# Kernel optimization log

Hardware: AMD Instinct MI355X
Metric: run time of the kernel (lower is better)

The kernel has to match this reference:

```python
import jax, jax.numpy as jnp
import numpy as np

B, H, W, C = 4, 64, 64, 512
EPS = 1e-3  # keras BatchNormalization default epsilon


def setup_inputs() -> dict:
    key = jax.random.key(0)
    ks = jax.random.split(key, 16)
    c8, c2 = C // 8, C // 2
    sc = lambda fan_in: 1.0 / np.sqrt(fan_in)
    inp = {
        "x": jax.random.normal(ks[0], (B, H, W, C), dtype=jnp.float32),
        # 1x1 conv weights as [Cin, Cout] matrices
        "wf": jax.random.normal(ks[1], (C, c8), dtype=jnp.float32) * sc(C),
        "bf": jnp.zeros((c8,), jnp.float32),
        "wg": jax.random.normal(ks[2], (C, c8), dtype=jnp.float32) * sc(C),
        "bg": jnp.zeros((c8,), jnp.float32),
        "wh": jax.random.normal(ks[3], (C, c2), dtype=jnp.float32) * sc(C),
        "bh": jnp.zeros((c2,), jnp.float32),
        "wo": jax.random.normal(ks[4], (c2, C), dtype=jnp.float32) * sc(c2),
        "bo": jnp.zeros((C,), jnp.float32),
        "gamma": jax.random.normal(ks[5], (1,), dtype=jnp.float32) * 0.05,
        # concat 1x1 conv (2C -> C), has bias (use_batchnorm=False default)
        "wc": jax.random.normal(ks[6], (2 * C, C), dtype=jnp.float32) * sc(2 * C),
        "bc": jnp.zeros((C,), jnp.float32),
        # BN inference params (moving statistics)
        "bn_scale": jnp.ones((C,), jnp.float32),
        "bn_bias": jnp.zeros((C,), jnp.float32),
        "bn_mean": jnp.zeros((C,), jnp.float32),
        "bn_var": jnp.ones((C,), jnp.float32),
    }
    return inp


def reference(x, wf, bf, wg, bg, wh, bh, wo, bo, gamma, wc, bc,
              bn_scale, bn_bias, bn_mean, bn_var):
    b, h, w, c = x.shape
    n = h * w
    xf = x.reshape(b, n, c)
    f = xf @ wf + bf          # [B, N, C/8]
    g = xf @ wg + bg          # [B, N, C/8]
    hv = xf @ wh + bh         # [B, N, C/2]
    s = jnp.einsum('bnd,bmd->bnm', g, f)   # [B, N, N]
    beta = jax.nn.softmax(s, axis=-1)
    o = jnp.einsum('bnm,bmd->bnd', beta, hv)  # [B, N, C/2]
    o = o @ wo + bo                            # [B, N, C]
    att = gamma * o + xf                       # gamma-scaled residual
    cat = jnp.concatenate([att, xf], axis=-1)  # [B, N, 2C]
    y = cat @ wc + bc
    # BatchNorm inference + relu
    y = (y - bn_mean) * (bn_scale / jnp.sqrt(bn_var + EPS)) + bn_bias
    y = jax.nn.relu(y)
    return y.reshape(b, h, w, c)
```

## Files before the change

kernel.cpp:

```cpp
#include <hip/hip_runtime.h>
#include <hip/hip_bf16.h>

typedef __bf16 bf16x8 __attribute__((ext_vector_type(8)));
typedef float f32x4 __attribute__((ext_vector_type(4)));

#define EPSBN 1e-3f

constexpr int NPIX = 4096;
constexpr int D2 = 256;

__global__ __launch_bounds__(256) void k_cvt(const float* __restrict__ x,
                                             __bf16* __restrict__ xb, int n4) {
  int i = blockIdx.x * 256 + threadIdx.x;
  if (i >= n4) return;
  float4 v = reinterpret_cast<const float4*>(x)[i];
  union { __bf16 h[4]; uint2 u; } o;
  o.h[0] = (__bf16)v.x; o.h[1] = (__bf16)v.y; o.h[2] = (__bf16)v.z; o.h[3] = (__bf16)v.w;
  reinterpret_cast<uint2*>(xb)[i] = o.u;
}

__global__ __launch_bounds__(256) void kp_wfgh(const float* __restrict__ wf,
                                               const float* __restrict__ wg,
                                               const float* __restrict__ wh,
                                               __bf16* __restrict__ WT) {
  int idx = blockIdx.x * 256 + threadIdx.x;
  int c = idx >> 9, k = idx & 511;
  float v = (c < 64) ? wf[k * 64 + c] : (c < 128) ? wg[k * 64 + (c - 64)] : wh[k * 256 + (c - 128)];
  WT[idx] = (__bf16)v;
}

__global__ __launch_bounds__(128) void kp_bias384(const float* bf_, const float* bg_,
                                                  const float* bh_, float* bias) {
  int c = blockIdx.x * 128 + threadIdx.x;
  bias[c] = (c < 64) ? bf_[c] : (c < 128) ? bg_[c - 64] : bh_[c - 128];
}

__global__ __launch_bounds__(256) void kp_wow(const float* __restrict__ wo,
                                              const float* __restrict__ wc,
                                              float* __restrict__ Wow) {
  int idx = blockIdx.x * 256 + threadIdx.x;
  int d = idx >> 9, c = idx & 511;
  float acc = 0.f;
  for (int j = 0; j < 512; ++j) acc += wo[d * 512 + j] * wc[j * 512 + c];
  Wow[idx] = acc;
}

__global__ __launch_bounds__(256) void kp_wcat(const float* __restrict__ Wow,
                                               const float* __restrict__ wc,
                                               const float* __restrict__ gamma,
                                               const float* __restrict__ bns,
                                               const float* __restrict__ bnv,
                                               __bf16* __restrict__ WT) {
  int idx = blockIdx.x * 256 + threadIdx.x;
  int c = idx / 768, k = idx % 768;
  float s = bns[c] * rsqrtf(bnv[c] + EPSBN);
  float v;
  if (k < 256) v = gamma[0] * Wow[k * 512 + c] * s;
  else { int kk = k - 256; v = (wc[kk * 512 + c] + wc[(512 + kk) * 512 + c]) * s; }
  WT[idx] = (__bf16)v;
}

__global__ __launch_bounds__(256) void kp_biasF(const float* bo, const float* wc, const float* bc,
                                                const float* gamma, const float* bns, const float* bnb,
                                                const float* bnm, const float* bnv, float* biasF) {
  int c = blockIdx.x * 256 + threadIdx.x;
  float s = bns[c] * rsqrtf(bnv[c] + EPSBN);
  float acc = 0.f;
  for (int j = 0; j < 512; ++j) acc += bo[j] * wc[j * 512 + c];
  float pre = bc[c] + gamma[0] * acc;
  biasF[c] = (pre - bnm[c]) * s + bnb[c];
}

template <int KT, int NC, bool FINAL>
__global__ __launch_bounds__(256) void k_gemm(const __bf16* __restrict__ A1, int k1, int lda1,
                                              const __bf16* __restrict__ A2, int lda2,
                                              const __bf16* __restrict__ WT,
                                              const float* __restrict__ bias,
                                              void* __restrict__ outp) {
  __shared__ __bf16 As[128][72];
  __shared__ __bf16 Ws[64][72];
  const int m0 = blockIdx.x * 128, n0 = blockIdx.y * 64;
  const int tid = threadIdx.x, lane = tid & 63, w = tid >> 6;
  const int wr = w >> 1, wcl = w & 1;
  const int l15 = lane & 15, l4 = lane >> 4;
  f32x4 acc[4][2] = {};
  for (int ks = 0; ks < KT; ks += 64) {
    const __bf16* Asrc; int lda, kb;
    if (ks < k1) { Asrc = A1; lda = lda1; kb = ks; }
    else         { Asrc = A2; lda = lda2; kb = ks - k1; }
#pragma unroll
    for (int it = 0; it < 4; ++it) {
      int idx = it * 256 + tid, r = idx >> 3, ch = idx & 7;
      *(bf16x8*)(&As[r][ch * 8]) = *(const bf16x8*)(Asrc + (size_t)(m0 + r) * lda + kb + ch * 8);
    }
#pragma unroll
    for (int it = 0; it < 2; ++it) {
      int idx = it * 256 + tid, r = idx >> 3, ch = idx & 7;
      *(bf16x8*)(&Ws[r][ch * 8]) = *(const bf16x8*)(WT + (size_t)(n0 + r) * KT + ks + ch * 8);
    }
    __syncthreads();
#pragma unroll
    for (int kk = 0; kk < 2; ++kk) {
      int krd = kk * 32 + l4 * 8;
      bf16x8 av[4], bv[2];
#pragma unroll
      for (int mi = 0; mi < 4; ++mi) av[mi] = *(const bf16x8*)(&As[wr * 64 + mi * 16 + l15][krd]);
#pragma unroll
      for (int ni = 0; ni < 2; ++ni) bv[ni] = *(const bf16x8*)(&Ws[wcl * 32 + ni * 16 + l15][krd]);
#pragma unroll
      for (int mi = 0; mi < 4; ++mi)
#pragma unroll
        for (int ni = 0; ni < 2; ++ni)
          acc[mi][ni] = __builtin_amdgcn_mfma_f32_16x16x32_bf16(av[mi], bv[ni], acc[mi][ni], 0, 0, 0);
    }
    __syncthreads();
  }
#pragma unroll
  for (int mi = 0; mi < 4; ++mi)
#pragma unroll
    for (int ni = 0; ni < 2; ++ni) {
      int col = n0 + wcl * 32 + ni * 16 + l15;
      float bcol = bias[col];
#pragma unroll
      for (int r = 0; r < 4; ++r) {
        int row = m0 + wr * 64 + mi * 16 + l4 * 4 + r;
        float v = acc[mi][ni][r] + bcol;
        if (FINAL) ((float*)outp)[(size_t)row * NC + col] = fmaxf(v, 0.f);
        else ((__bf16*)outp)[(size_t)row * NC + col] = (__bf16)v;
      }
    }
}

__global__ __launch_bounds__(256) void k_trans(const __bf16* __restrict__ fgh,
                                               __bf16* __restrict__ hvT) {
  __shared__ __bf16 T[64][72];
  int b = blockIdx.z, n0 = blockIdx.x * 64, d0 = blockIdx.y * 64;
  int tid = threadIdx.x;
  const __bf16* src = fgh + (size_t)b * NPIX * 384;
#pragma unroll
  for (int it = 0; it < 2; ++it) {
    int idx = it * 256 + tid, r = idx >> 3, ch = idx & 7;
    *(bf16x8*)(&T[r][ch * 8]) = *(const bf16x8*)(src + (size_t)(n0 + r) * 384 + 128 + d0 + ch * 8);
  }
  __syncthreads();
  __bf16* dst = hvT + ((size_t)b * D2 + d0) * NPIX + n0;
#pragma unroll
  for (int it = 0; it < 2; ++it) {
    int idx = it * 256 + tid, r = idx >> 3, ch = idx & 7;
    bf16x8 v;
#pragma unroll
    for (int j = 0; j < 8; ++j) v[j] = T[ch * 8 + j][r];
    *(bf16x8*)(dst + (size_t)r * NPIX + ch * 8) = v;
  }
}

__global__ __launch_bounds__(256, 2) void k_attn(const __bf16* __restrict__ fgh,
                                                 const __bf16* __restrict__ hvT,
                                                 __bf16* __restrict__ obuf) {
  __shared__ __bf16 Fs[64][72];
  __shared__ __bf16 Vs[256][72];
  __shared__ __bf16 Ps[32][72];
  __shared__ float Lp[4][32];
  const int b = blockIdx.y, q0 = blockIdx.x * 32;
  const int tid = threadIdx.x, w = tid >> 6, lane = tid & 63;
  const int l15 = lane & 15, l4 = lane >> 4;
  const __bf16* base = fgh + (size_t)b * NPIX * 384;
  const __bf16* vbase = hvT + (size_t)b * D2 * NPIX;
  bf16x8 aG[2][2];
#pragma unroll
  for (int qi = 0; qi < 2; ++qi)
#pragma unroll
    for (int kk = 0; kk < 2; ++kk)
      aG[qi][kk] = *(const bf16x8*)(base + (size_t)(q0 + qi * 16 + l15) * 384 + 64 + kk * 32 + l4 * 8);
  f32x4 accO[2][4] = {};
  f32x4 lsum[2] = {};
  for (int m0 = 0; m0 < NPIX; m0 += 64) {
#pragma unroll
    for (int it = 0; it < 2; ++it) {
      int idx = it * 256 + tid, r = idx >> 3, ch = idx & 7;
      *(bf16x8*)(&Fs[r][ch * 8]) = *(const bf16x8*)(base + (size_t)(m0 + r) * 384 + ch * 8);
    }
#pragma unroll
    for (int it = 0; it < 8; ++it) {
      int idx = it * 256 + tid, r = idx >> 3, ch = idx & 7;
      *(bf16x8*)(&Vs[r][ch * 8]) = *(const bf16x8*)(vbase + (size_t)r * NPIX + m0 + ch * 8);
    }
    __syncthreads();
#pragma unroll
    for (int qi = 0; qi < 2; ++qi) {
      f32x4 sa = {};
#pragma unroll
      for (int kk = 0; kk < 2; ++kk) {
        bf16x8 bF = *(const bf16x8*)(&Fs[w * 16 + l15][kk * 32 + l4 * 8]);
        sa = __builtin_amdgcn_mfma_f32_16x16x32_bf16(aG[qi][kk], bF, sa, 0, 0, 0);
      }
#pragma unroll
      for (int r = 0; r < 4; ++r) {
        float p = __expf(sa[r]);
        lsum[qi][r] += p;
        Ps[qi * 16 + l4 * 4 + r][w * 16 + l15] = (__bf16)p;
      }
    }
    __syncthreads();
#pragma unroll
    for (int kk = 0; kk < 2; ++kk) {
      bf16x8 aP[2];
#pragma unroll
      for (int qi = 0; qi < 2; ++qi) aP[qi] = *(const bf16x8*)(&Ps[qi * 16 + l15][kk * 32 + l4 * 8]);
#pragma unroll
      for (int dj = 0; dj < 4; ++dj) {
        bf16x8 bV = *(const bf16x8*)(&Vs[w * 64 + dj * 16 + l15][kk * 32 + l4 * 8]);
#pragma unroll
        for (int qi = 0; qi < 2; ++qi)
          accO[qi][dj] = __builtin_amdgcn_mfma_f32_16x16x32_bf16(aP[qi], bV, accO[qi][dj], 0, 0, 0);
      }
    }
    __syncthreads();
  }
#pragma unroll
  for (int qi = 0; qi < 2; ++qi)
#pragma unroll
    for (int r = 0; r < 4; ++r) {
      float v = lsum[qi][r];
      v += __shfl_xor(v, 1); v += __shfl_xor(v, 2); v += __shfl_xor(v, 4); v += __shfl_xor(v, 8);
      lsum[qi][r] = v;
    }
  if (l15 == 0) {
#pragma unroll
    for (int qi = 0; qi < 2; ++qi)
#pragma unroll
      for (int r = 0; r < 4; ++r) Lp[w][qi * 16 + l4 * 4 + r] = lsum[qi][r];
  }
  __syncthreads();
  __bf16* out = obuf + ((size_t)b * NPIX + q0) * D2;
#pragma unroll
  for (int qi = 0; qi < 2; ++qi)
#pragma unroll
    for (int r = 0; r < 4; ++r) {
      int q = qi * 16 + l4 * 4 + r;
      float lt = Lp[0][q] + Lp[1][q] + Lp[2][q] + Lp[3][q];
      float inv = 1.0f / lt;
#pragma unroll
      for (int dj = 0; dj < 4; ++dj)
        out[(size_t)q * D2 + w * 64 + dj * 16 + l15] = (__bf16)(accO[qi][dj][r] * inv);
    }
}

extern "C" void kernel_launch(void* const* d_in, const int* in_sizes, int n_in,
                              void* d_out, int out_size, void* d_ws, size_t ws_size,
                              hipStream_t stream) {
  const float* x = (const float*)d_in[0];
  const float* wf = (const float*)d_in[1];
  const float* bf_ = (const float*)d_in[2];
  const float* wg = (const float*)d_in[3];
  const float* bg_ = (const float*)d_in[4];
  const float* wh = (const float*)d_in[5];
  const float* bh_ = (const float*)d_in[6];
  const float* wo = (const float*)d_in[7];
  const float* bo = (const float*)d_in[8];
  const float* gamma = (const float*)d_in[9];
  const float* wc = (const float*)d_in[10];
  const float* bc = (const float*)d_in[11];
  const float* bns = (const float*)d_in[12];
  const float* bnb = (const float*)d_in[13];
  const float* bnm = (const float*)d_in[14];
  const float* bnv = (const float*)d_in[15];
  (void)in_sizes; (void)n_in; (void)out_size; (void)ws_size;

  char* ws = (char*)d_ws;
  __bf16* xb     = (__bf16*)(ws + 0);
  __bf16* fgh    = (__bf16*)(ws + 16777216);
  __bf16* hvT    = (__bf16*)(ws + 29360128);
  __bf16* obuf   = (__bf16*)(ws + 37748736);
  __bf16* WfghT  = (__bf16*)(ws + 46137344);
  float*  bias384= (float*) (ws + 46530560);
  float*  Wow    = (float*) (ws + 46532096);
  __bf16* WcatT  = (__bf16*)(ws + 47056384);
  float*  biasF  = (float*) (ws + 47842816);
  float* out = (float*)d_out;

  hipLaunchKernelGGL(k_cvt, dim3(8192), dim3(256), 0, stream, x, xb, 2097152);
  hipLaunchKernelGGL(kp_wfgh, dim3(768), dim3(256), 0, stream, wf, wg, wh, WfghT);
  hipLaunchKernelGGL(kp_bias384, dim3(3), dim3(128), 0, stream, bf_, bg_, bh_, bias384);
  hipLaunchKernelGGL(kp_wow, dim3(512), dim3(256), 0, stream, wo, wc, Wow);
  hipLaunchKernelGGL(kp_wcat, dim3(1536), dim3(256), 0, stream, Wow, wc, gamma, bns, bnv, WcatT);
  hipLaunchKernelGGL(kp_biasF, dim3(2), dim3(256), 0, stream, bo, wc, bc, gamma, bns, bnb, bnm, bnv, biasF);
  hipLaunchKernelGGL((k_gemm<512, 384, false>), dim3(128, 6), dim3(256), 0, stream,
                     xb, 512, 512, xb, 512, WfghT, bias384, (void*)fgh);
  hipLaunchKernelGGL(k_trans, dim3(64, 4, 4), dim3(256), 0, stream, fgh, hvT);
  hipLaunchKernelGGL(k_attn, dim3(128, 4), dim3(256), 0, stream, fgh, hvT, obuf);
  hipLaunchKernelGGL((k_gemm<768, 512, true>), dim3(128, 8), dim3(256), 0, stream,
                     obuf, 256, 256, xb, 512, WcatT, biasF, (void*)out);
}
```

Measured before the change: 302.4 us.

## Fuse hv transpose into projection GEMM and restructure attention to register-resident operands

The projection GEMM now writes f/g into a compact 128-wide buffer and writes hv directly transposed, which removes the separate transpose kernel and its extra pass over memory. The attention kernel is rewritten to use 512 threads per 64-query block. It keeps F and V fragments in registers, prefetched from global memory one tile ahead, instead of staging them through shared memory. Only the probability tile goes through a double-buffered LDS array, synchronised by a single raw barrier per step, and blocks are mapped so each XCD handles one batch. The cost is higher register pressure, scattered 8-byte transposed stores in the GEMM epilogue, and a reliance on L2 for the repeated global fragment loads.

Result: faster. 278.4 us (-7.9%).

```diff
diff --git a/kernel.cpp b/kernel.cpp
--- a/kernel.cpp
+++ b/kernel.cpp
@@ -8,6 +8,12 @@
 
 constexpr int NPIX = 4096;
 constexpr int D2 = 256;
+
+#define RAW_BARRIER() do { \
+  asm volatile("s_waitcnt lgkmcnt(0)" ::: "memory"); \
+  __builtin_amdgcn_s_barrier(); \
+  asm volatile("" ::: "memory"); \
+} while (0)
 
 __global__ __launch_bounds__(256) void k_cvt(const float* __restrict__ x,
                                              __bf16* __restrict__ xb, int n4) {
@@ -71,12 +77,13 @@
   biasF[c] = (pre - bnm[c]) * s + bnb[c];
 }
 
-template <int KT, int NC, bool FINAL>
+template <int KT, int NC, int MODE>
 __global__ __launch_bounds__(256) void k_gemm(const __bf16* __restrict__ A1, int k1, int lda1,
                                               const __bf16* __restrict__ A2, int lda2,
                                               const __bf16* __restrict__ WT,
                                               const float* __restrict__ bias,
-                                              void* __restrict__ outp) {
+                                              void* __restrict__ out1,
+                                              void* __restrict__ out2) {
   __shared__ __bf16 As[128][72];
   __shared__ __bf16 Ws[64][72];
   const int m0 = blockIdx.x * 128, n0 = blockIdx.y * 64;
@@ -121,129 +128,142 @@
     for (int ni = 0; ni < 2; ++ni) {
       int col = n0 + wcl * 32 + ni * 16 + l15;
       float bcol = bias[col];
-#pragma unroll
-      for (int r = 0; r < 4; ++r) {
-        int row = m0 + wr * 64 + mi * 16 + l4 * 4 + r;
-        float v = acc[mi][ni][r] + bcol;
-        if (FINAL) ((float*)outp)[(size_t)row * NC + col] = fmaxf(v, 0.f);
-        else ((__bf16*)outp)[(size_t)row * NC + col] = (__bf16)v;
+      int row0 = m0 + wr * 64 + mi * 16 + l4 * 4;
+      if (MODE == 1) {
+        float* out = (float*)out1;
+#pragma unroll
+        for (int r = 0; r < 4; ++r)
+          out[(size_t)(row0 + r) * NC + col] = fmaxf(acc[mi][ni][r] + bcol, 0.f);
+      } else {
+        if (col < 128) {
+          __bf16* fg = (__bf16*)out1;
+#pragma unroll
+          for (int r = 0; r < 4; ++r)
+            fg[(size_t)(row0 + r) * 128 + col] = (__bf16)(acc[mi][ni][r] + bcol);
+        } else {
+          __bf16* hvT = (__bf16*)out2;
+          int bb = row0 >> 12, n = row0 & 4095;
+          union { __bf16 h[4]; uint2 u; } pk;
+#pragma unroll
+          for (int r = 0; r < 4; ++r) pk.h[r] = (__bf16)(acc[mi][ni][r] + bcol);
+          *(uint2*)(hvT + ((size_t)(bb * 256 + (col - 128))) * 4096 + n) = pk.u;
+        }
       }
     }
 }
 
-__global__ __launch_bounds__(256) void k_trans(const __bf16* __restrict__ fgh,
-                                               __bf16* __restrict__ hvT) {
-  __shared__ __bf16 T[64][72];
-  int b = blockIdx.z, n0 = blockIdx.x * 64, d0 = blockIdx.y * 64;
-  int tid = threadIdx.x;
-  const __bf16* src = fgh + (size_t)b * NPIX * 384;
-#pragma unroll
-  for (int it = 0; it < 2; ++it) {
-    int idx = it * 256 + tid, r = idx >> 3, ch = idx & 7;
-    *(bf16x8*)(&T[r][ch * 8]) = *(const bf16x8*)(src + (size_t)(n0 + r) * 384 + 128 + d0 + ch * 8);
+__global__ __launch_bounds__(512, 2) void k_attn(const __bf16* __restrict__ fg,
+                                                 const __bf16* __restrict__ hvT,
+                                                 __bf16* __restrict__ obuf) {
+  __shared__ __bf16 PsT[2][64][136];
+  __shared__ float Lp[8][64];
+  const int id = blockIdx.x;
+  const int xcd = id & 7, i2 = id >> 3;
+  const int b = xcd >> 1;
+  const int q0 = (i2 * 2 + (xcd & 1)) * 64;
+  const int tid = threadIdx.x, w = tid >> 6, lane = tid & 63;
+  const int l15 = lane & 15, l4 = lane >> 4;
+  const __bf16* fgb = fg + (size_t)b * NPIX * 128;
+  const __bf16* vb = hvT + (size_t)b * D2 * NPIX;
+
+  bf16x8 bG[4][2];
+#pragma unroll
+  for (int qt = 0; qt < 4; ++qt)
+#pragma unroll
+    for (int kk = 0; kk < 2; ++kk)
+      bG[qt][kk] = *(const bf16x8*)(fgb + (size_t)(q0 + qt * 16 + l15) * 128 + 64 + kk * 32 + l4 * 8);
+
+  bf16x8 aF[2], bV[2][4];
+#pragma unroll
+  for (int kk = 0; kk < 2; ++kk)
+    aF[kk] = *(const bf16x8*)(fgb + (size_t)(w * 16 + l15) * 128 + kk * 32 + l4 * 8);
+#pragma unroll
+  for (int dj = 0; dj < 2; ++dj)
+#pragma unroll
+    for (int k4 = 0; k4 < 4; ++k4)
+      bV[dj][k4] = *(const bf16x8*)(vb + (size_t)(w * 32 + dj * 16 + l15) * NPIX + k4 * 32 + l4 * 8);
+
+  f32x4 accO[4][2] = {};
+  float lsum[4] = {0.f, 0.f, 0.f, 0.f};
+
+  for (int t = 0; t < 32; ++t) {
+    const int mn = ((t + 1) * 128) & (NPIX - 1);
+    const int bufi = t & 1;
+    f32x4 s[4];
+#pragma unroll
+    for (int qt = 0; qt < 4; ++qt) {
+      s[qt] = (f32x4){0.f, 0.f, 0.f, 0.f};
+#pragma unroll
+      for (int kk = 0; kk < 2; ++kk)
+        s[qt] = __builtin_amdgcn_mfma_f32_16x16x32_bf16(aF[kk], bG[qt][kk], s[qt], 0, 0, 0);
+    }
+    bf16x8 aFn[2];
+#pragma unroll
+    for (int kk = 0; kk < 2; ++kk)
+      aFn[kk] = *(const bf16x8*)(fgb + (size_t)(mn + w * 16 + l15) * 128 + kk * 32 + l4 * 8);
+#pragma unroll
+    for (int qt = 0; qt < 4; ++qt) {
+      float p0 = __expf(s[qt][0]), p1 = __expf(s[qt][1]);
+      float p2 = __expf(s[qt][2]), p3 = __expf(s[qt][3]);
+      lsum[qt] += (p0 + p1) + (p2 + p3);
+      union { __bf16 h[2]; uint u; } w0, w1;
+      w0.h[0] = (__bf16)p0; w0.h[1] = (__bf16)p1;
+      w1.h[0] = (__bf16)p2; w1.h[1] = (__bf16)p3;
+      *(uint*)(&PsT[bufi][qt * 16 + l15][w * 16 + l4 * 4]) = w0.u;
+      *(uint*)(&PsT[bufi][qt * 16 + l15][w * 16 + l4 * 4 + 2]) = w1.u;
+    }
+    RAW_BARRIER();
+#pragma unroll
+    for (int qt = 0; qt < 4; ++qt) {
+      bf16x8 aP[4];
+#pragma unroll
+      for (int k4 = 0; k4 < 4; ++k4)
+        aP[k4] = *(const bf16x8*)(&PsT[bufi][qt * 16 + l15][k4 * 32 + l4 * 8]);
+#pragma unroll
+      for (int dj = 0; dj < 2; ++dj)
+#pragma unroll
+        for (int k4 = 0; k4 < 4; ++k4)
+          accO[qt][dj] = __builtin_amdgcn_mfma_f32_16x16x32_bf16(aP[k4], bV[dj][k4], accO[qt][dj], 0, 0, 0);
+    }
+#pragma unroll
+    for (int dj = 0; dj < 2; ++dj)
+#pragma unroll
+      for (int k4 = 0; k4 < 4; ++k4)
+        bV[dj][k4] = *(const bf16x8*)(vb + (size_t)(w * 32 + dj * 16 + l15) * NPIX + mn + k4 * 32 + l4 * 8);
+    aF[0] = aFn[0]; aF[1] = aFn[1];
+  }
+
+#pragma unroll
+  for (int qt = 0; qt < 4; ++qt) {
+    float v = lsum[qt];
+    v += __shfl_xor(v, 16); v += __shfl_xor(v, 32);
+    lsum[qt] = v;
+  }
+  if (l4 == 0) {
+#pragma unroll
+    for (int qt = 0; qt < 4; ++qt) Lp[w][qt * 16 + l15] = lsum[qt];
   }
   __syncthreads();
-  __bf16* dst = hvT + ((size_t)b * D2 + d0) * NPIX + n0;
-#pragma unroll
-  for (int it = 0; it < 2; ++it) {
-    int idx = it * 256 + tid, r = idx >> 3, ch = idx & 7;
-    bf16x8 v;
-#pragma unroll
-    for (int j = 0; j < 8; ++j) v[j] = T[ch * 8 + j][r];
-    *(bf16x8*)(dst + (size_t)r * NPIX + ch * 8) = v;
-  }
-}
-
-__global__ __launch_bounds__(256, 2) void k_attn(const __bf16* __restrict__ fgh,
-                                                 const __bf16* __restrict__ hvT,
-                                                 __bf16* __restrict__ obuf) {
-  __shared__ __bf16 Fs[64][72];
-  __shared__ __bf16 Vs[256][72];
-  __shared__ __bf16 Ps[32][72];
-  __shared__ float Lp[4][32];
-  const int b = blockIdx.y, q0 = blockIdx.x * 32;
-  const int tid = threadIdx.x, w = tid >> 6, lane = tid & 63;
-  const int l15 = lane & 15, l4 = lane >> 4;
-  const __bf16* base = fgh + (size_t)b * NPIX * 384;
-  const __bf16* vbase = hvT + (size_t)b * D2 * NPIX;
-  bf16x8 aG[2][2];
-#pragma unroll
-  for (int qi = 0; qi < 2; ++qi)
-#pragma unroll
-    for (int kk = 0; kk < 2; ++kk)
-      aG[qi][kk] = *(const bf16x8*)(base + (size_t)(q0 + qi * 16 + l15) * 384 + 64 + kk * 32 + l4 * 8);
-  f32x4 accO[2][4] = {};
-  f32x4 lsum[2] = {};
-  for (int m0 = 0; m0 < NPIX; m0 += 64) {
-#pragma unroll
-    for (int it = 0; it < 2; ++it) {
-      int idx = it * 256 + tid, r = idx >> 3, ch = idx & 7;
-      *(bf16x8*)(&Fs[r][ch * 8]) = *(const bf16x8*)(base + (size_t)(m0 + r) * 384 + ch * 8);
-    }
-#pragma unroll
-    for (int it = 0; it < 8; ++it) {
-      int idx = it * 256 + tid, r = idx >> 3, ch = idx & 7;
-      *(bf16x8*)(&Vs[r][ch * 8]) = *(const bf16x8*)(vbase + (size_t)r * NPIX + m0 + ch * 8);
-    }
-    __syncthreads();
-#pragma unroll
-    for (int qi = 0; qi < 2; ++qi) {
-      f32x4 sa = {};
-#pragma unroll
-      for (int kk = 0; kk < 2; ++kk) {
-        bf16x8 bF = *(const bf16x8*)(&Fs[w * 16 + l15][kk * 32 + l4 * 8]);
-        sa = __builtin_amdgcn_mfma_f32_16x16x32_bf16(aG[qi][kk], bF, sa, 0, 0, 0);
-      }
-#pragma unroll
-      for (int r = 0; r < 4; ++r) {
-        float p = __expf(sa[r]);
-        lsum[qi][r] += p;
-        Ps[qi * 16 + l4 * 4 + r][w * 16 + l15] = (__bf16)p;
-      }
-    }
-    __syncthreads();
-#pragma unroll
-    for (int kk = 0; kk < 2; ++kk) {
-      bf16x8 aP[2];
-#pragma unroll
-      for (int qi = 0; qi < 2; ++qi) aP[qi] = *(const bf16x8*)(&Ps[qi * 16 + l15][kk * 32 + l4 * 8]);
-#pragma unroll
-      for (int dj = 0; dj < 4; ++dj) {
-        bf16x8 bV = *(const bf16x8*)(&Vs[w * 64 + dj * 16 + l15][kk * 32 + l4 * 8]);
-#pragma unroll
-        for (int qi = 0; qi < 2; ++qi)
-          accO[qi][dj] = __builtin_amdgcn_mfma_f32_16x16x32_bf16(aP[qi], bV, accO[qi][dj], 0, 0, 0);
-      }
-    }
-    __syncthreads();
-  }
-#pragma unroll
-  for (int qi = 0; qi < 2; ++qi)
+  float inv[4][4];
+#pragma unroll
+  for (int qt = 0; qt < 4; ++qt)
 #pragma unroll
     for (int r = 0; r < 4; ++r) {
-      float v = lsum[qi][r];
-      v += __shfl_xor(v, 1); v += __shfl_xor(v, 2); v += __shfl_xor(v, 4); v += __shfl_xor(v, 8);
-      lsum[qi][r] = v;
-    }
-  if (l15 == 0) {
-#pragma unroll
-    for (int qi = 0; qi < 2; ++qi)
-#pragma unroll
-      for (int r = 0; r < 4; ++r) Lp[w][qi * 16 + l4 * 4 + r] = lsum[qi][r];
-  }
-  __syncthreads();
-  __bf16* out = obuf + ((size_t)b * NPIX + q0) * D2;
-#pragma unroll
-  for (int qi = 0; qi < 2; ++qi)
-#pragma unroll
-    for (int r = 0; r < 4; ++r) {
-      int q = qi * 16 + l4 * 4 + r;
-      float lt = Lp[0][q] + Lp[1][q] + Lp[2][q] + Lp[3][q];
-      float inv = 1.0f / lt;
-#pragma unroll
-      for (int dj = 0; dj < 4; ++dj)
-        out[(size_t)q * D2 + w * 64 + dj * 16 + l15] = (__bf16)(accO[qi][dj][r] * inv);
-    }
+      int q = qt * 16 + l4 * 4 + r;
+      float lt = 0.f;
+#pragma unroll
+      for (int ww = 0; ww < 8; ++ww) lt += Lp[ww][q];
+      inv[qt][r] = 1.0f / lt;
+    }
+  __bf16* ob = obuf + ((size_t)b * NPIX + q0) * D2;
+#pragma unroll
+  for (int qt = 0; qt < 4; ++qt)
+#pragma unroll
+    for (int dj = 0; dj < 2; ++dj)
+#pragma unroll
+      for (int r = 0; r < 4; ++r)
+        ob[(size_t)(qt * 16 + l4 * 4 + r) * D2 + w * 32 + dj * 16 + l15] =
+            (__bf16)(accO[qt][dj][r] * inv[qt][r]);
 }
 
 extern "C" void kernel_launch(void* const* d_in, const int* in_sizes, int n_in,
@@ -269,14 +289,14 @@
 
   char* ws = (char*)d_ws;
   __bf16* xb     = (__bf16*)(ws + 0);
-  __bf16* fgh    = (__bf16*)(ws + 16777216);
-  __bf16* hvT    = (__bf16*)(ws + 29360128);
-  __bf16* obuf   = (__bf16*)(ws + 37748736);
-  __bf16* WfghT  = (__bf16*)(ws + 46137344);
-  float*  bias384= (float*) (ws + 46530560);
-  float*  Wow    = (float*) (ws + 46532096);
-  __bf16* WcatT  = (__bf16*)(ws + 47056384);
-  float*  biasF  = (float*) (ws + 47842816);
+  __bf16* fg     = (__bf16*)(ws + 16777216);
+  __bf16* hvT    = (__bf16*)(ws + 20971520);
+  __bf16* obuf   = (__bf16*)(ws + 29360128);
+  __bf16* WfghT  = (__bf16*)(ws + 37748736);
+  float*  bias384= (float*) (ws + 38141952);
+  float*  Wow    = (float*) (ws + 38143488);
+  __bf16* WcatT  = (__bf16*)(ws + 38667776);
+  float*  biasF  = (float*) (ws + 39454208);
   float* out = (float*)d_out;
 
   hipLaunchKernelGGL(k_cvt, dim3(8192), dim3(256), 0, stream, x, xb, 2097152);
@@ -285,10 +305,9 @@
   hipLaunchKernelGGL(kp_wow, dim3(512), dim3(256), 0, stream, wo, wc, Wow);
   hipLaunchKernelGGL(kp_wcat, dim3(1536), dim3(256), 0, stream, Wow, wc, gamma, bns, bnv, WcatT);
   hipLaunchKernelGGL(kp_biasF, dim3(2), dim3(256), 0, stream, bo, wc, bc, gamma, bns, bnb, bnm, bnv, biasF);
-  hipLaunchKernelGGL((k_gemm<512, 384, false>), dim3(128, 6), dim3(256), 0, stream,
-                     xb, 512, 512, xb, 512, WfghT, bias384, (void*)fgh);
-  hipLaunchKernelGGL(k_trans, dim3(64, 4, 4), dim3(256), 0, stream, fgh, hvT);
-  hipLaunchKernelGGL(k_attn, dim3(128, 4), dim3(256), 0, stream, fgh, hvT, obuf);
-  hipLaunchKernelGGL((k_gemm<768, 512, true>), dim3(128, 8), dim3(256), 0, stream,
-                     obuf, 256, 256, xb, 512, WcatT, biasF, (void*)out);
-}
+  hipLaunchKernelGGL((k_gemm<512, 384, 0>), dim3(128, 6), dim3(256), 0, stream,
+                     xb, 512, 512, xb, 512, WfghT, bias384, (void*)fg, (void*)hvT);
+  hipLaunchKernelGGL(k_attn, dim3(256), dim3(512), 0, stream, fg, hvT, obuf);
+  hipLaunchKernelGGL((k_gemm<768, 512, 1>), dim3(128, 8), dim3(256), 0, stream,
+                     obuf, 256, 256, xb, 512, WcatT, biasF, (void*)out, nullptr);
+}
```
